# Performance work log

Measured on AMD Instinct MI355X. Metric: run time of the kernel, lower is better.

## Reference

```python
import jax, jax.numpy as jnp
import numpy as np

N_NODES = 50000


def setup_inputs() -> dict:
    key = jax.random.key(0)
    ks = jax.random.split(key, 5)
    d_in, d_out = 96, 96
    x = jax.random.normal(ks[0], (N_NODES, d_in), dtype=jnp.float32)
    edge_index = jax.random.randint(ks[1], (2, 800000), 0, N_NODES, dtype=jnp.int64)
    W_gcn = jax.random.normal(ks[2], (d_in, d_out), dtype=jnp.float32) / np.sqrt(d_in)
    b_gcn = jnp.zeros((d_out,), dtype=jnp.float32)
    W_lin = jax.random.normal(ks[3], (d_in, d_out), dtype=jnp.float32) / np.sqrt(d_in)
    b_lin = jnp.zeros((d_out,), dtype=jnp.float32)
    return {"x": x, "edge_index": edge_index, "W_gcn": W_gcn, "b_gcn": b_gcn,
            "W_lin": W_lin, "b_lin": b_lin}


def mish(y):
    return y * jnp.tanh(jax.nn.softplus(y))


def gcn_conv(x, edge_index, W, b):
    n = x.shape[0]
    # add self-loops (PyG GCNConv default)
    loop = jnp.arange(n, dtype=edge_index.dtype)
    src = jnp.concatenate([edge_index[0], loop])  # [E+N]
    dst = jnp.concatenate([edge_index[1], loop])
    h = x @ W  # [N, d_out]
    # symmetric normalization: deg over destination nodes of A+I
    deg = jax.ops.segment_sum(jnp.ones_like(dst, dtype=h.dtype), dst, num_segments=n)
    dinv = jnp.where(deg > 0, jax.lax.rsqrt(deg), 0.0)
    norm = dinv[src] * dinv[dst]  # [E+N]
    msg = h[src] * norm[:, None]  # gather + scale
    agg = jax.ops.segment_sum(msg, dst, num_segments=n)  # scatter-add
    return agg + b


def reference(x, edge_index, W_gcn, b_gcn, W_lin, b_lin):
    x_gcn = gcn_conv(x, edge_index, W_gcn, b_gcn)
    x_skip = x @ W_lin + b_lin
    return mish(x_gcn + x_skip)
```

## Files before the change

kernel.cpp:

```cpp
#include <hip/hip_runtime.h>
#include <hip/hip_bf16.h>
#include <math.h>

#define D 96
#define CAP 48
#define NXCD 8
#define FILL_GPB 80

typedef __attribute__((ext_vector_type(8))) short bf16x8;
typedef __attribute__((ext_vector_type(4))) float f32x4;
typedef __attribute__((ext_vector_type(8))) unsigned short u16x8;

__global__ __launch_bounds__(256) void prep_kernel(const float* __restrict__ Wg,
                                                   const float* __restrict__ Wl,
                                                   __hip_bfloat16* __restrict__ wT,
                                                   int* __restrict__ cursor, int n) {
    int i = blockIdx.x * 256 + threadIdx.x;
    if (i < n) cursor[i] = 0;
    if (i < 192 * D) {
        int c = i / D, k = i % D;
        float v = (c < D) ? Wg[k * D + c] : Wl[k * D + (c - D)];
        wT[i] = __float2bfloat16(v);
    }
}

__global__ __launch_bounds__(256) void fill_bucket_kernel(
    const int* __restrict__ src, const int* __restrict__ dst,
    int* __restrict__ cursor, unsigned short* __restrict__ bucket,
    int e, int n)
{
    int g = blockIdx.x & (NXCD - 1);
    int bc = blockIdx.x >> 3;
    int lo = (g * n) / NXCD;
    int hi = ((g + 1) * n) / NXCD;
    int stride = FILL_GPB * 256;
    for (int i = bc * 256 + threadIdx.x; i < e; i += stride) {
        int d = dst[i];
        if (d >= lo && d < hi) {
            int pos = atomicAdd(&cursor[d], 1);
            if (pos < CAP) bucket[(size_t)d * CAP + pos] = (unsigned short)src[i];
        }
    }
}

__global__ __launch_bounds__(256) void gemm_mfma_kernel(
    const float* __restrict__ x, const __hip_bfloat16* __restrict__ wT,
    const float* __restrict__ bl, const int* __restrict__ cursor,
    __hip_bfloat16* __restrict__ hp, float* __restrict__ out, int n)
{
    __shared__ __hip_bfloat16 sx[64 * D];
    __shared__ __hip_bfloat16 sw[192 * D];
    int tid = threadIdx.x;
    int rbase = blockIdx.x * 64;

    {
        const ushort4* s4 = (const ushort4*)wT;
        ushort4* d4 = (ushort4*)sw;
        for (int i = tid; i < 192 * D / 4; i += 256) d4[i] = s4[i];
    }
    for (int i = tid; i < 64 * D / 4; i += 256) {
        int r = i / (D / 4);
        int c4 = (i % (D / 4)) * 4;
        int grow = rbase + r;
        float4 v = make_float4(0.f, 0.f, 0.f, 0.f);
        if (grow < n) v = *(const float4*)&x[(size_t)grow * D + c4];
        __hip_bfloat16* dp = &sx[r * D + c4];
        dp[0] = __float2bfloat16(v.x); dp[1] = __float2bfloat16(v.y);
        dp[2] = __float2bfloat16(v.z); dp[3] = __float2bfloat16(v.w);
    }
    __syncthreads();

    int w = tid >> 6, l = tid & 63;
    int lrow = l & 15, lk = (l >> 4) * 8;

    bf16x8 a[3];
#pragma unroll
    for (int kc = 0; kc < 3; kc++)
        a[kc] = *(const bf16x8*)&sx[(w * 16 + lrow) * D + kc * 32 + lk];

    f32x4 acc[12];
#pragma unroll
    for (int ct = 0; ct < 12; ct++) acc[ct] = (f32x4){0.f, 0.f, 0.f, 0.f};

#pragma unroll
    for (int ct = 0; ct < 12; ct++) {
#pragma unroll
        for (int kc = 0; kc < 3; kc++) {
            bf16x8 b = *(const bf16x8*)&sw[(ct * 16 + lrow) * D + kc * 32 + lk];
            acc[ct] = __builtin_amdgcn_mfma_f32_16x16x32_bf16(a[kc], b, acc[ct], 0, 0, 0);
        }
    }

    int col0 = l & 15;
#pragma unroll
    for (int j = 0; j < 4; j++) {
        int row = rbase + w * 16 + (l >> 4) * 4 + j;
        if (row < n) {
            float dinv = rsqrtf((float)(cursor[row] + 1));
            size_t hb = (size_t)row * D;
#pragma unroll
            for (int ct = 0; ct < 6; ct++)
                hp[hb + ct * 16 + col0] = __float2bfloat16(acc[ct][j] * dinv);
#pragma unroll
            for (int ct = 0; ct < 6; ct++) {
                int c = ct * 16 + col0;
                out[hb + c] = acc[6 + ct][j] + bl[c];
            }
        }
    }
}

__device__ __forceinline__ float mish_f(float v) {
    float u = __expf(v);
    float t = u * u + 2.f * u;
    float m = v * t / (t + 2.f);
    return (v > 30.f) ? v : m;
}

__global__ __launch_bounds__(256) void gather_kernel(
    const __hip_bfloat16* __restrict__ hp, const int* __restrict__ cursor,
    const unsigned short* __restrict__ bucket, const float* __restrict__ bg,
    float* __restrict__ out, int n)
{
    int tid = threadIdx.x;
    int g = tid >> 5;
    int lane = tid & 31;
    int sub = lane >> 4;
    int j = lane & 15;
    bool active = (j < 12);
    int d = blockIdx.x * 8 + g;
    if (d >= n) return;

    int deg = cursor[d];
    int cnt = deg < CAP ? deg : CAP;
    const unsigned short* bk = bucket + (size_t)d * CAP;
    const unsigned short* hpu = (const unsigned short*)hp;

    float a0[8], a1[8], a2[8], a3[8];
#pragma unroll
    for (int k = 0; k < 8; k++) { a0[k] = 0.f; a1[k] = 0.f; a2[k] = 0.f; a3[k] = 0.f; }

    if (sub == 0 && active) {
        u16x8 v = *(const u16x8*)&hpu[(size_t)d * D + j * 8];
#pragma unroll
        for (int k = 0; k < 8; k++)
            a0[k] += __uint_as_float(((unsigned int)v[k]) << 16);
    }

    int e = sub;
    for (; e + 6 < cnt; e += 8) {
        int s0 = bk[e], s1 = bk[e + 2], s2 = bk[e + 4], s3 = bk[e + 6];
        if (active) {
            u16x8 v0 = *(const u16x8*)&hpu[(size_t)s0 * D + j * 8];
            u16x8 v1 = *(const u16x8*)&hpu[(size_t)s1 * D + j * 8];
            u16x8 v2 = *(const u16x8*)&hpu[(size_t)s2 * D + j * 8];
            u16x8 v3 = *(const u16x8*)&hpu[(size_t)s3 * D + j * 8];
#pragma unroll
            for (int k = 0; k < 8; k++) {
                a0[k] += __uint_as_float(((unsigned int)v0[k]) << 16);
                a1[k] += __uint_as_float(((unsigned int)v1[k]) << 16);
                a2[k] += __uint_as_float(((unsigned int)v2[k]) << 16);
                a3[k] += __uint_as_float(((unsigned int)v3[k]) << 16);
            }
        }
    }
    for (; e < cnt; e += 2) {
        int s0 = bk[e];
        if (active) {
            u16x8 v0 = *(const u16x8*)&hpu[(size_t)s0 * D + j * 8];
#pragma unroll
            for (int k = 0; k < 8; k++)
                a0[k] += __uint_as_float(((unsigned int)v0[k]) << 16);
        }
    }

#pragma unroll
    for (int k = 0; k < 8; k++) a0[k] += (a1[k] + a2[k]) + a3[k];
#pragma unroll
    for (int k = 0; k < 8; k++) a0[k] += __shfl_xor(a0[k], 16, 32);

    if (sub == 0 && active) {
        float dinv = rsqrtf((float)(deg + 1));
        size_t ob = (size_t)d * D + j * 8;
        float4 s0 = *(const float4*)&out[ob];
        float4 s1 = *(const float4*)&out[ob + 4];
        float4 b0 = *(const float4*)&bg[j * 8];
        float4 b1 = *(const float4*)&bg[j * 8 + 4];
        float r[8];
        r[0] = mish_f(a0[0] * dinv + b0.x + s0.x);
        r[1] = mish_f(a0[1] * dinv + b0.y + s0.y);
        r[2] = mish_f(a0[2] * dinv + b0.z + s0.z);
        r[3] = mish_f(a0[3] * dinv + b0.w + s0.w);
        r[4] = mish_f(a0[4] * dinv + b1.x + s1.x);
        r[5] = mish_f(a0[5] * dinv + b1.y + s1.y);
        r[6] = mish_f(a0[6] * dinv + b1.z + s1.z);
        r[7] = mish_f(a0[7] * dinv + b1.w + s1.w);
        *(float4*)&out[ob]     = make_float4(r[0], r[1], r[2], r[3]);
        *(float4*)&out[ob + 4] = make_float4(r[4], r[5], r[6], r[7]);
    }
}

extern "C" void kernel_launch(void* const* d_in, const int* in_sizes, int n_in,
                              void* d_out, int out_size, void* d_ws, size_t ws_size,
                              hipStream_t stream)
{
    const float* x  = (const float*)d_in[0];
    const int* edge = (const int*)d_in[1];
    const float* Wg = (const float*)d_in[2];
    const float* bg = (const float*)d_in[3];
    const float* Wl = (const float*)d_in[4];
    const float* bl = (const float*)d_in[5];
    float* out = (float*)d_out;

    const int n = in_sizes[0] / D;
    const int e = in_sizes[1] / 2;
    const int* src = edge;
    const int* dst = edge + e;

    int* cursor = (int*)d_ws;
    size_t off_b = ((size_t)n * sizeof(int) + 255) & ~(size_t)255;
    __hip_bfloat16* wT = (__hip_bfloat16*)((char*)d_ws + off_b);
    off_b += (size_t)192 * D * sizeof(__hip_bfloat16);
    off_b = (off_b + 255) & ~(size_t)255;
    __hip_bfloat16* hp = (__hip_bfloat16*)((char*)d_ws + off_b);
    off_b += (size_t)n * D * sizeof(__hip_bfloat16);
    off_b = (off_b + 255) & ~(size_t)255;
    unsigned short* bucket = (unsigned short*)((char*)d_ws + off_b);

    int prep_blocks = (n + 255) / 256;
    prep_kernel<<<prep_blocks, 256, 0, stream>>>(Wg, Wl, wT, cursor, n);
    fill_bucket_kernel<<<NXCD * FILL_GPB, 256, 0, stream>>>(src, dst, cursor, bucket, e, n);
    gemm_mfma_kernel<<<(n + 63) / 64, 256, 0, stream>>>(x, wT, bl, cursor, hp, out, n);
    gather_kernel<<<(n + 7) / 8, 256, 0, stream>>>(hp, cursor, bucket, bg, out, n);
}
```

Before: 179.6 us.

## Load GEMM A-fragments directly from global memory and widen bucket fill grid

The GEMM kernel drops its shared-memory staging of x and has each lane load its bf16 A-fragment straight from global memory as float4 pairs. This removes an LDS write/read round-trip and shrinks shared memory use, which may allow more blocks per CU. The bucket fill kernel doubles its grid size, uses nontemporal loads for the edge arrays, and reads src only for edges that fall in the block's destination range. The tradeoff is that global reads for x become less coalesced per lane, and more fill blocks may raise atomic contention.

```diff
diff --git a/kernel.cpp b/kernel.cpp
--- a/kernel.cpp
+++ b/kernel.cpp
@@ -5,7 +5,7 @@
 #define D 96
 #define CAP 48
 #define NXCD 8
-#define FILL_GPB 80
+#define FILL_GPB 160
 
 typedef __attribute__((ext_vector_type(8))) short bf16x8;
 typedef __attribute__((ext_vector_type(4))) float f32x4;
@@ -35,10 +35,11 @@
     int hi = ((g + 1) * n) / NXCD;
     int stride = FILL_GPB * 256;
     for (int i = bc * 256 + threadIdx.x; i < e; i += stride) {
-        int d = dst[i];
+        int d = __builtin_nontemporal_load(&dst[i]);
         if (d >= lo && d < hi) {
+            int s = __builtin_nontemporal_load(&src[i]);
             int pos = atomicAdd(&cursor[d], 1);
-            if (pos < CAP) bucket[(size_t)d * CAP + pos] = (unsigned short)src[i];
+            if (pos < CAP) bucket[(size_t)d * CAP + pos] = (unsigned short)s;
         }
     }
 }
@@ -48,7 +49,6 @@
     const float* __restrict__ bl, const int* __restrict__ cursor,
     __hip_bfloat16* __restrict__ hp, float* __restrict__ out, int n)
 {
-    __shared__ __hip_bfloat16 sx[64 * D];
     __shared__ __hip_bfloat16 sw[192 * D];
     int tid = threadIdx.x;
     int rbase = blockIdx.x * 64;
@@ -58,25 +58,30 @@
         ushort4* d4 = (ushort4*)sw;
         for (int i = tid; i < 192 * D / 4; i += 256) d4[i] = s4[i];
     }
-    for (int i = tid; i < 64 * D / 4; i += 256) {
-        int r = i / (D / 4);
-        int c4 = (i % (D / 4)) * 4;
-        int grow = rbase + r;
-        float4 v = make_float4(0.f, 0.f, 0.f, 0.f);
-        if (grow < n) v = *(const float4*)&x[(size_t)grow * D + c4];
-        __hip_bfloat16* dp = &sx[r * D + c4];
-        dp[0] = __float2bfloat16(v.x); dp[1] = __float2bfloat16(v.y);
-        dp[2] = __float2bfloat16(v.z); dp[3] = __float2bfloat16(v.w);
-    }
-    __syncthreads();
 
     int w = tid >> 6, l = tid & 63;
     int lrow = l & 15, lk = (l >> 4) * 8;
+    int arow = rbase + w * 16 + lrow;
 
     bf16x8 a[3];
-#pragma unroll
-    for (int kc = 0; kc < 3; kc++)
-        a[kc] = *(const bf16x8*)&sx[(w * 16 + lrow) * D + kc * 32 + lk];
+    if (arow < n) {
+        const float* xr = &x[(size_t)arow * D];
+#pragma unroll
+        for (int kc = 0; kc < 3; kc++) {
+            float4 u = *(const float4*)&xr[kc * 32 + lk];
+            float4 v = *(const float4*)&xr[kc * 32 + lk + 4];
+            __hip_bfloat16 t[8];
+            t[0] = __float2bfloat16(u.x); t[1] = __float2bfloat16(u.y);
+            t[2] = __float2bfloat16(u.z); t[3] = __float2bfloat16(u.w);
+            t[4] = __float2bfloat16(v.x); t[5] = __float2bfloat16(v.y);
+            t[6] = __float2bfloat16(v.z); t[7] = __float2bfloat16(v.w);
+            a[kc] = *(const bf16x8*)t;
+        }
+    } else {
+#pragma unroll
+        for (int kc = 0; kc < 3; kc++) a[kc] = (bf16x8){0,0,0,0,0,0,0,0};
+    }
+    __syncthreads();
 
     f32x4 acc[12];
 #pragma unroll
```

Result: faster. 169.9 us (-5.4%).
